# Kernel optimization log

Hardware: AMD Instinct MI355X
Metric: run time of the kernel (lower is better)

The kernel has to match this reference:

```python
import jax, jax.numpy as jnp
import numpy as np

E, H, PV, RD, NS, SP, T = 4, 64, 300, 64, 8, 6, 2
N = 5000
IN_GRU = 2 * E * H  # 512


def layer_norm(x, g, b, eps=1e-5):
    m = jnp.mean(x, axis=-1, keepdims=True)
    v = jnp.var(x, axis=-1, keepdims=True)
    return (x - m) * jax.lax.rsqrt(v + eps) * g + b


def setup_inputs() -> dict:
    key = jax.random.key(0)
    ks = jax.random.split(key, 32)
    s = 0.05
    inp = {
        'adjacency_matrix': (jax.random.uniform(ks[0], (E, N, N), jnp.float32) < 0.01).astype(jnp.float32),
        'node_states': jax.random.normal(ks[1], (N, NS), jnp.float32),
        'node_ids': jnp.arange(N, dtype=jnp.int32),
        'node_vectors': jax.random.normal(ks[2], (N, PV), jnp.float32),
        'node_size_and_pos': jax.random.normal(ks[3], (N, SP), jnp.float32),
        # reduce_dimentionality: Linear(300,64)+Tanh
        'W_red': jax.random.normal(ks[4], (PV, RD), jnp.float32) * s,
        'b_red': jnp.zeros((RD,), jnp.float32),
        # node_init2hidden: Linear(64+8+6,64)+Tanh
        'W_init': jax.random.normal(ks[5], (RD + NS + SP, H), jnp.float32) * s,
        'b_init': jnp.zeros((H,), jnp.float32),
        # per-edge-type message FCs (stacked over edge types)
        'W_out': jax.random.normal(ks[6], (E, H, H), jnp.float32) * s,
        'b_out': jnp.zeros((E, H), jnp.float32),
        'W_in_e': jax.random.normal(ks[7], (E, H, H), jnp.float32) * s,
        'b_in_e': jnp.zeros((E, H), jnp.float32),
        # LayerNormGRUCell(2*E*H, H)
        'W_ih_rz': jax.random.normal(ks[8], (IN_GRU, 2 * H), jnp.float32) * s,
        'b_ih_rz': jnp.zeros((2 * H,), jnp.float32),
        'W_hh_rz': jax.random.normal(ks[9], (H, 2 * H), jnp.float32) * s,
        'b_hh_rz': jnp.zeros((2 * H,), jnp.float32),
        'W_ih_c': jax.random.normal(ks[10], (IN_GRU, H), jnp.float32) * s,
        'b_ih_c': jnp.zeros((H,), jnp.float32),
        'W_hh_c': jax.random.normal(ks[11], (H, H), jnp.float32) * s,
        'b_hh_c': jnp.zeros((H,), jnp.float32),
        'g_i2h': jnp.ones((2 * H,), jnp.float32), 'be_i2h': jnp.zeros((2 * H,), jnp.float32),
        'g_h2h': jnp.ones((2 * H,), jnp.float32), 'be_h2h': jnp.zeros((2 * H,), jnp.float32),
        'g_ci': jnp.ones((H,), jnp.float32), 'be_ci': jnp.zeros((H,), jnp.float32),
        'g_ch': jnp.ones((H,), jnp.float32), 'be_ch': jnp.zeros((H,), jnp.float32),
    }
    return inp


def _messages(A, h, W, b):
    # per-edge-type FC + tanh: [E,N,H]
    hs = jnp.tanh(jnp.einsum('nh,ehk->enk', h, W) + b[:, None, :])
    # adjacency matmul per edge type: [E,N,N] @ [E,N,H] -> [E,N,H]
    m = jnp.einsum('enm,emh->enh', A, hs)
    # torch.stack(list,1).view(N,-1) == [N, E*H]
    return jnp.transpose(m, (1, 0, 2)).reshape(h.shape[0], E * H)


def reference(adjacency_matrix, node_states, node_ids, node_vectors, node_size_and_pos,
              W_red, b_red, W_init, b_init, W_out, b_out, W_in_e, b_in_e,
              W_ih_rz, b_ih_rz, W_hh_rz, b_hh_rz, W_ih_c, b_ih_c, W_hh_c, b_hh_c,
              g_i2h, be_i2h, g_h2h, be_h2h, g_ci, be_ci, g_ch, be_ch):
    emb = jnp.tanh(node_vectors @ W_red + b_red)                      # [N,RD]
    node_init = jnp.concatenate([emb, node_states, node_size_and_pos], axis=1)
    h = jnp.tanh(node_init @ W_init + b_init)                          # [N,H]
    A_out = adjacency_matrix
    A_in = jnp.transpose(adjacency_matrix, (0, 2, 1))
    for _ in range(T):
        m_out = _messages(A_out, h, W_out, b_out)                      # [N,E*H]
        m_in = _messages(A_in, h, W_in_e, b_in_e)                      # [N,E*H]
        msg = jnp.concatenate([m_out, m_in], axis=1)                   # [N,2EH]
        # LayerNormGRUCell
        rz = jax.nn.sigmoid(layer_norm(msg @ W_ih_rz + b_ih_rz, g_i2h, be_i2h)
                            + layer_norm(h @ W_hh_rz + b_hh_rz, g_h2h, be_h2h))
        r, z = rz[:, :H], rz[:, H:]
        c = jnp.tanh(layer_norm(msg @ W_ih_c + b_ih_c, g_ci, be_ci)
                     + r * layer_norm(h @ W_hh_c + b_hh_c, g_ch, be_ch))
        h = z * h + (1.0 - z) * c
    return h
```

## Files before the change

kernel.cpp:

```cpp
#include <hip/hip_runtime.h>
#include <math.h>

#define N    5000
#define E    4
#define H    64
#define PV   300
#define RD   64
#define NS_  8
#define SP_  6
#define NI   (RD + NS_ + SP_)
#define GH   (2 * H)
#define MSGW (2 * E * H)
#define CAP  128
#define NPB  8
#define MSG_BPS 256

#define PK_S0 ((MSGW / 4) * GH)
#define PK_S1 ((MSGW / 4) * H)
#define PK_S2 ((H / 4) * GH)
#define PK_S3 ((H / 4) * H)
#define PK_TOT (PK_S0 + PK_S1 + PK_S2 + PK_S3)

__device__ __forceinline__ float wsum(float v) {
    v += __shfl_xor(v, 32, 64);
    v += __shfl_xor(v, 16, 64);
    v += __shfl_xor(v, 8, 64);
    v += __shfl_xor(v, 4, 64);
    v += __shfl_xor(v, 2, 64);
    v += __shfl_xor(v, 1, 64);
    return v;
}

__global__ __launch_bounds__(256) void k_zero(int4* __restrict__ p) {
    const int i = blockIdx.x * 256 + threadIdx.x;
    if (i < (2 * E * N) / 4) p[i] = make_int4(0, 0, 0, 0);
}

__global__ __launch_bounds__(256) void k_pack(
    const float* __restrict__ Wih_rz, const float* __restrict__ Wih_c,
    const float* __restrict__ Whh_rz, const float* __restrict__ Whh_c,
    float4* __restrict__ Prz, float4* __restrict__ Pc,
    float4* __restrict__ Phrz, float4* __restrict__ Phc)
{
    const int i = blockIdx.x * 256 + threadIdx.x;
    if (i < PK_S0) {
        const int kq = i / GH, col = i - kq * GH;
        Prz[i] = make_float4(Wih_rz[(4 * kq + 0) * GH + col],
                             Wih_rz[(4 * kq + 1) * GH + col],
                             Wih_rz[(4 * kq + 2) * GH + col],
                             Wih_rz[(4 * kq + 3) * GH + col]);
    } else if (i < PK_S0 + PK_S1) {
        const int t = i - PK_S0;
        const int kq = t / H, col = t - kq * H;
        Pc[t] = make_float4(Wih_c[(4 * kq + 0) * H + col],
                            Wih_c[(4 * kq + 1) * H + col],
                            Wih_c[(4 * kq + 2) * H + col],
                            Wih_c[(4 * kq + 3) * H + col]);
    } else if (i < PK_S0 + PK_S1 + PK_S2) {
        const int t = i - PK_S0 - PK_S1;
        const int kq = t / GH, col = t - kq * GH;
        Phrz[t] = make_float4(Whh_rz[(4 * kq + 0) * GH + col],
                              Whh_rz[(4 * kq + 1) * GH + col],
                              Whh_rz[(4 * kq + 2) * GH + col],
                              Whh_rz[(4 * kq + 3) * GH + col]);
    } else if (i < PK_TOT) {
        const int t = i - PK_S0 - PK_S1 - PK_S2;
        const int kq = t / H, col = t - kq * H;
        Phc[t] = make_float4(Whh_c[(4 * kq + 0) * H + col],
                             Whh_c[(4 * kq + 1) * H + col],
                             Whh_c[(4 * kq + 2) * H + col],
                             Whh_c[(4 * kq + 3) * H + col]);
    }
}

__global__ __launch_bounds__(64) void k_init(
    const float* __restrict__ NV, const float* __restrict__ NSt,
    const float* __restrict__ SPos, const float* __restrict__ Wred,
    const float* __restrict__ bred, const float* __restrict__ Winit,
    const float* __restrict__ binit, float* __restrict__ h)
{
    __shared__ float nv[4 * PV];
    __shared__ float ni[4 * NI];
    const int n0 = blockIdx.x * 4;
    const int j = threadIdx.x;

    for (int idx = j; idx < 4 * PV; idx += 64) nv[idx] = NV[(size_t)n0 * PV + idx];
    __syncthreads();

    float acc[4];
    {
        const float br = bred[j];
        #pragma unroll
        for (int nn = 0; nn < 4; ++nn) acc[nn] = br;
    }
    for (int k = 0; k < PV; ++k) {
        const float w = Wred[k * RD + j];
        #pragma unroll
        for (int nn = 0; nn < 4; ++nn) acc[nn] += nv[nn * PV + k] * w;
    }
    #pragma unroll
    for (int nn = 0; nn < 4; ++nn) ni[nn * NI + j] = tanhf(acc[nn]);
    if (j < NS_) {
        #pragma unroll
        for (int nn = 0; nn < 4; ++nn) ni[nn * NI + RD + j] = NSt[(size_t)(n0 + nn) * NS_ + j];
    }
    if (j < SP_) {
        #pragma unroll
        for (int nn = 0; nn < 4; ++nn) ni[nn * NI + RD + NS_ + j] = SPos[(size_t)(n0 + nn) * SP_ + j];
    }
    __syncthreads();

    float a2[4];
    {
        const float bi = binit[j];
        #pragma unroll
        for (int nn = 0; nn < 4; ++nn) a2[nn] = bi;
    }
    for (int k = 0; k < NI; ++k) {
        const float w = Winit[k * H + j];
        #pragma unroll
        for (int nn = 0; nn < 4; ++nn) a2[nn] += ni[nn * NI + k] * w;
    }
    #pragma unroll
    for (int nn = 0; nn < 4; ++nn) h[(size_t)(n0 + nn) * H + j] = tanhf(a2[nn]);
}

__global__ __launch_bounds__(256) void k_build(
    const float* __restrict__ A, int* __restrict__ cnt_out, int* __restrict__ cnt_in,
    unsigned short* __restrict__ idx_out, unsigned short* __restrict__ idx_in)
{
    const int r = blockIdx.x;
    const int e = r / N;
    const int n = r - e * N;
    __shared__ int s_cnt;
    __shared__ int s_cols[CAP];
    if (threadIdx.x == 0) s_cnt = 0;
    __syncthreads();

    const float4* row = (const float4*)(A + (size_t)r * N);
    const int lane = threadIdx.x & 63;
    #pragma unroll
    for (int it = 0; it < 5; ++it) {
        const int c = threadIdx.x + it * 256;
        float4 v = make_float4(0.f, 0.f, 0.f, 0.f);
        if (c < N / 4) v = row[c];
        #pragma unroll
        for (int comp = 0; comp < 4; ++comp) {
            const float val = (comp == 0) ? v.x : (comp == 1) ? v.y : (comp == 2) ? v.z : v.w;
            const bool p = (val != 0.f);
            const unsigned long long m = __ballot(p);
            if (m) {
                int base = 0;
                if (lane == 0) base = atomicAdd(&s_cnt, (int)__popcll(m));
                base = __shfl(base, 0, 64);
                if (p) {
                    const int pos = base + (int)__popcll(m & ((1ull << lane) - 1ull));
                    if (pos < CAP) s_cols[pos] = 4 * c + comp;
                }
            }
        }
    }
    __syncthreads();
    const int cnt = min(s_cnt, CAP);
    if (threadIdx.x == 0) cnt_out[r] = cnt;
    for (int i = threadIdx.x; i < cnt; i += 256)
        idx_out[(size_t)r * CAP + i] = (unsigned short)s_cols[i];
    for (int i = threadIdx.x; i < cnt; i += 256) {
        const int m = s_cols[i];
        const int p = atomicAdd(&cnt_in[e * N + m], 1);
        if (p < CAP) idx_in[(size_t)(e * N + m) * CAP + p] = (unsigned short)n;
    }
}

__global__ __launch_bounds__(256) void k_hs(
    const float* __restrict__ h, const float* __restrict__ Wout,
    const float* __restrict__ bout, const float* __restrict__ Win,
    const float* __restrict__ bin, float* __restrict__ hs_out,
    float* __restrict__ hs_in)
{
    __shared__ float hsd[8 * H];
    const int n0 = blockIdx.x * 8;
    const int tid = threadIdx.x;
    const int e = tid >> 6, j = tid & 63;

    for (int idx = tid; idx < 8 * H; idx += 256) hsd[idx] = h[(size_t)n0 * H + idx];
    __syncthreads();

    float aO[8], aI[8];
    {
        const float bO = bout[e * H + j], bI = bin[e * H + j];
        #pragma unroll
        for (int nn = 0; nn < 8; ++nn) { aO[nn] = bO; aI[nn] = bI; }
    }
    for (int k = 0; k < H; ++k) {
        const float wo = Wout[(e * H + k) * H + j];
        const float wi = Win[(e * H + k) * H + j];
        #pragma unroll
        for (int nn = 0; nn < 8; ++nn) {
            const float hv = hsd[nn * H + k];
            aO[nn] += hv * wo;
            aI[nn] += hv * wi;
        }
    }
    #pragma unroll
    for (int nn = 0; nn < 8; ++nn) {
        hs_out[((size_t)e * N + n0 + nn) * H + j] = tanhf(aO[nn]);
        hs_in[((size_t)e * N + n0 + nn) * H + j]  = tanhf(aI[nn]);
    }
}

__global__ __launch_bounds__(256) void k_msg(
    const float* __restrict__ hs_out, const float* __restrict__ hs_in,
    const int* __restrict__ cnt_out, const int* __restrict__ cnt_in,
    const unsigned short* __restrict__ idx_out, const unsigned short* __restrict__ idx_in,
    float* __restrict__ msg)
{
    const int slice = blockIdx.x & 7;
    const int sb = blockIdx.x >> 3;
    const int dir = slice >> 2;
    const int e = slice & 3;
    const int tid = threadIdx.x;
    const int wv = tid >> 6;
    const int lane = tid & 63;
    const int g = lane >> 4;
    const int l = lane & 15;

    const float4* hs4 = (const float4*)((dir ? hs_in : hs_out) + (size_t)e * N * H);
    const int* cnt = (dir ? cnt_in : cnt_out) + e * N;
    const unsigned short* idx = (dir ? idx_in : idx_out) + (size_t)e * N * CAP;
    float4* mdst = (float4*)msg;

    for (int n = sb * 4 + wv; n < N; n += MSG_BPS * 4) {
        const int c = min(cnt[n], CAP);
        const unsigned short* lst = idx + (size_t)n * CAP;

        float ax = 0.f, ay = 0.f, az = 0.f, aw = 0.f;
        int i = g;
        for (; i + 12 < c; i += 16) {
            const int m0 = lst[i];
            const int m1 = lst[i + 4];
            const int m2 = lst[i + 8];
            const int m3 = lst[i + 12];
            const float4 v0 = hs4[(size_t)m0 * (H / 4) + l];
            const float4 v1 = hs4[(size_t)m1 * (H / 4) + l];
            const float4 v2 = hs4[(size_t)m2 * (H / 4) + l];
            const float4 v3 = hs4[(size_t)m3 * (H / 4) + l];
            ax += (v0.x + v1.x) + (v2.x + v3.x);
            ay += (v0.y + v1.y) + (v2.y + v3.y);
            az += (v0.z + v1.z) + (v2.z + v3.z);
            aw += (v0.w + v1.w) + (v2.w + v3.w);
        }
        for (; i < c; i += 4) {
            const float4 v = hs4[(size_t)lst[i] * (H / 4) + l];
            ax += v.x; ay += v.y; az += v.z; aw += v.w;
        }

        ax += __shfl_xor(ax, 16, 64); ay += __shfl_xor(ay, 16, 64);
        az += __shfl_xor(az, 16, 64); aw += __shfl_xor(aw, 16, 64);
        ax += __shfl_xor(ax, 32, 64); ay += __shfl_xor(ay, 32, 64);
        az += __shfl_xor(az, 32, 64); aw += __shfl_xor(aw, 32, 64);

        if (g == 0) {
            mdst[(size_t)n * (MSGW / 4) + dir * (E * H / 4) + e * (H / 4) + l] =
                make_float4(ax, ay, az, aw);
        }
    }
}

__global__ __launch_bounds__(256) void k_gru(
    const float* __restrict__ msg, const float* __restrict__ h,
    const float4* __restrict__ Prz, const float4* __restrict__ Pc,
    const float4* __restrict__ Phrz, const float4* __restrict__ Phc,
    const float* __restrict__ bih_rz, const float* __restrict__ bhh_rz,
    const float* __restrict__ bih_c, const float* __restrict__ bhh_c,
    const float* __restrict__ g_i2h, const float* __restrict__ be_i2h,
    const float* __restrict__ g_h2h, const float* __restrict__ be_h2h,
    const float* __restrict__ g_ci, const float* __restrict__ be_ci,
    const float* __restrict__ g_ch, const float* __restrict__ be_ch,
    float* __restrict__ h_out)
{
    __shared__ float pb[2][64][12];
    const int n0 = blockIdx.x * NPB;
    const int tid = threadIdx.x;
    const int j = tid & 63;
    const int wv = __builtin_amdgcn_readfirstlane(tid >> 6);
    const int kh = wv & 1;
    const int q  = wv >> 1;
    const int nb = q * 4;

    const float4* ms4 = (const float4*)msg;
    const float4* hg4 = (const float4*)h;

    float a0[4], a1[4], c0[4];
    {
        const float v0 = kh ? 0.f : bih_rz[j];
        const float v1 = kh ? 0.f : bih_rz[H + j];
        const float vc = kh ? 0.f : bih_c[j];
        #pragma unroll
        for (int i = 0; i < 4; ++i) { a0[i] = v0; a1[i] = v1; c0[i] = vc; }
    }
    {
        const int kq0 = kh * (MSGW / 8);
        #pragma unroll 2
        for (int t = 0; t < MSGW / 8; ++t) {
            const int kq = kq0 + t;
            const float4 w0 = Prz[kq * GH + j];
            const float4 w1 = Prz[kq * GH + 64 + j];
            const float4 wc = Pc[kq * H + j];
            #pragma unroll
            for (int i = 0; i < 4; ++i) {
                const float4 m = ms4[(size_t)(n0 + nb + i) * (MSGW / 4) + kq];
                a0[i] += m.x * w0.x; a0[i] += m.y * w0.y;
                a0[i] += m.z * w0.z; a0[i] += m.w * w0.w;
                a1[i] += m.x * w1.x; a1[i] += m.y * w1.y;
                a1[i] += m.z * w1.z; a1[i] += m.w * w1.w;
                c0[i] += m.x * wc.x; c0[i] += m.y * wc.y;
                c0[i] += m.z * wc.z; c0[i] += m.w * wc.w;
            }
        }
    }

    float b0[4], b1[4], ch[4];
    {
        const float v0 = kh ? 0.f : bhh_rz[j];
        const float v1 = kh ? 0.f : bhh_rz[H + j];
        const float vc = kh ? 0.f : bhh_c[j];
        #pragma unroll
        for (int i = 0; i < 4; ++i) { b0[i] = v0; b1[i] = v1; ch[i] = vc; }
    }
    {
        const int kq0 = kh * (H / 8);
        #pragma unroll 2
        for (int t = 0; t < H / 8; ++t) {
            const int kq = kq0 + t;
            const float4 w0 = Phrz[kq * GH + j];
            const float4 w1 = Phrz[kq * GH + 64 + j];
            const float4 wc = Phc[kq * H + j];
            #pragma unroll
            for (int i = 0; i < 4; ++i) {
                const float4 m = hg4[(size_t)(n0 + nb + i) * (H / 4) + kq];
                b0[i] += m.x * w0.x; b0[i] += m.y * w0.y;
                b0[i] += m.z * w0.z; b0[i] += m.w * w0.w;
                b1[i] += m.x * w1.x; b1[i] += m.y * w1.y;
                b1[i] += m.z * w1.z; b1[i] += m.w * w1.w;
                ch[i] += m.x * wc.x; ch[i] += m.y * wc.y;
                ch[i] += m.z * wc.z; ch[i] += m.w * wc.w;
            }
        }
    }

    if (kh == 1) {
        #pragma unroll
        for (int i = 0; i < 4; ++i) {
            pb[q][j][i]     = a0[i];
            pb[q][j][4 + i] = a1[i];
            pb[q][j][8 + i] = c0[i];
        }
    }
    __syncthreads();
    if (kh == 0) {
        #pragma unroll
        for (int i = 0; i < 4; ++i) {
            a0[i] += pb[q][j][i];
            a1[i] += pb[q][j][4 + i];
            c0[i] += pb[q][j][8 + i];
        }
    }
    __syncthreads();
    if (kh == 1) {
        #pragma unroll
        for (int i = 0; i < 4; ++i) {
            pb[q][j][i]     = b0[i];
            pb[q][j][4 + i] = b1[i];
            pb[q][j][8 + i] = ch[i];
        }
    }
    __syncthreads();

    if (kh == 0) {
        #pragma unroll
        for (int i = 0; i < 4; ++i) {
            b0[i] += pb[q][j][i];
            b1[i] += pb[q][j][4 + i];
            ch[i] += pb[q][j][8 + i];
        }

        const float gi0 = g_i2h[j], gi1 = g_i2h[H + j], bi0 = be_i2h[j], bi1 = be_i2h[H + j];
        const float gh0 = g_h2h[j], gh1 = g_h2h[H + j], bh0 = be_h2h[j], bh1 = be_h2h[H + j];
        const float gci = g_ci[j], bci = be_ci[j], gchv = g_ch[j], bchv = be_ch[j];

        #pragma unroll
        for (int i = 0; i < 4; ++i) {
            float s  = wsum(a0[i] + a1[i]);
            float q_ = wsum(a0[i] * a0[i] + a1[i] * a1[i]);
            float mn = s * (1.f / GH);
            float vr = q_ * (1.f / GH) - mn * mn;
            float rs = rsqrtf(vr + 1e-5f);
            float x0 = (a0[i] - mn) * rs * gi0 + bi0;
            float x1 = (a1[i] - mn) * rs * gi1 + bi1;
            float s2  = wsum(b0[i] + b1[i]);
            float q2  = wsum(b0[i] * b0[i] + b1[i] * b1[i]);
            float mn2 = s2 * (1.f / GH);
            float vr2 = q2 * (1.f / GH) - mn2 * mn2;
            float rs2 = rsqrtf(vr2 + 1e-5f);
            float y0 = (b0[i] - mn2) * rs2 * gh0 + bh0;
            float y1 = (b1[i] - mn2) * rs2 * gh1 + bh1;
            const float r_ = 1.f / (1.f + expf(-(x0 + y0)));
            const float z_ = 1.f / (1.f + expf(-(x1 + y1)));

            float s3  = wsum(c0[i]);
            float q3  = wsum(c0[i] * c0[i]);
            float mn3 = s3 * (1.f / H);
            float vr3 = q3 * (1.f / H) - mn3 * mn3;
            float rs3 = rsqrtf(vr3 + 1e-5f);
            float xc = (c0[i] - mn3) * rs3 * gci + bci;
            float s4  = wsum(ch[i]);
            float q4  = wsum(ch[i] * ch[i]);
            float mn4 = s4 * (1.f / H);
            float vr4 = q4 * (1.f / H) - mn4 * mn4;
            float rs4 = rsqrtf(vr4 + 1e-5f);
            float hc = (ch[i] - mn4) * rs4 * gchv + bchv;
            float c  = tanhf(xc + r_ * hc);
            const int n = n0 + nb + i;
            const float hp = h[(size_t)n * H + j];
            h_out[(size_t)n * H + j] = z_ * hp + (1.f - z_) * c;
        }
    }
}

extern "C" void kernel_launch(void* const* d_in, const int* in_sizes, int n_in,
                              void* d_out, int out_size, void* d_ws, size_t ws_size,
                              hipStream_t stream)
{
    const float* A      = (const float*)d_in[0];
    const float* nstate = (const float*)d_in[1];
    const float* nvec   = (const float*)d_in[3];
    const float* nsp    = (const float*)d_in[4];
    const float* Wred   = (const float*)d_in[5];
    const float* bred   = (const float*)d_in[6];
    const float* Winit  = (const float*)d_in[7];
    const float* binit  = (const float*)d_in[8];
    const float* Wout   = (const float*)d_in[9];
    const float* bout   = (const float*)d_in[10];
    const float* Wine   = (const float*)d_in[11];
    const float* bine   = (const float*)d_in[12];
    const float* Wih_rz = (const float*)d_in[13];
    const float* bih_rz = (const float*)d_in[14];
    const float* Whh_rz = (const float*)d_in[15];
    const float* bhh_rz = (const float*)d_in[16];
    const float* Wih_c  = (const float*)d_in[17];
    const float* bih_c  = (const float*)d_in[18];
    const float* Whh_c  = (const float*)d_in[19];
    const float* bhh_c  = (const float*)d_in[20];
    const float* g_i2h  = (const float*)d_in[21];
    const float* be_i2h = (const float*)d_in[22];
    const float* g_h2h  = (const float*)d_in[23];
    const float* be_h2h = (const float*)d_in[24];
    const float* g_ci   = (const float*)d_in[25];
    const float* be_ci  = (const float*)d_in[26];
    const float* g_ch   = (const float*)d_in[27];
    const float* be_ch  = (const float*)d_in[28];

    char* ws = (char*)d_ws;
    size_t off = 0;
    auto alloc = [&](size_t bytes) {
        void* p = ws + off;
        off += (bytes + 255) & ~(size_t)255;
        return p;
    };
    float* h0  = (float*)alloc((size_t)N * H * 4);
    float* h1  = (float*)alloc((size_t)N * H * 4);
    float* hsO = (float*)alloc((size_t)E * N * H * 4);
    float* hsI = (float*)alloc((size_t)E * N * H * 4);
    float* msg = (float*)alloc((size_t)N * MSGW * 4);
    int* cnts  = (int*)alloc((size_t)2 * E * N * 4);
    int* cnt_out = cnts;
    int* cnt_in  = cnts + E * N;
    unsigned short* idxO = (unsigned short*)alloc((size_t)E * N * CAP * 2);
    unsigned short* idxI = (unsigned short*)alloc((size_t)E * N * CAP * 2);
    float4* Prz  = (float4*)alloc((size_t)PK_S0 * 16);
    float4* Pc   = (float4*)alloc((size_t)PK_S1 * 16);
    float4* Phrz = (float4*)alloc((size_t)PK_S2 * 16);
    float4* Phc  = (float4*)alloc((size_t)PK_S3 * 16);

    k_zero<<<(2 * E * N / 4 + 255) / 256, 256, 0, stream>>>((int4*)cnts);
    k_pack<<<(PK_TOT + 255) / 256, 256, 0, stream>>>(Wih_rz, Wih_c, Whh_rz, Whh_c,
                                                     Prz, Pc, Phrz, Phc);
    k_init<<<N / 4, 64, 0, stream>>>(nvec, nstate, nsp, Wred, bred, Winit, binit, h0);
    k_build<<<E * N, 256, 0, stream>>>(A, cnt_out, cnt_in, idxO, idxI);

    const float* hc = h0;
    for (int t = 0; t < 2; ++t) {
        k_hs<<<N / 8, 256, 0, stream>>>(hc, Wout, bout, Wine, bine, hsO, hsI);
        k_msg<<<8 * MSG_BPS, 256, 0, stream>>>(hsO, hsI, cnt_out, cnt_in, idxO, idxI, msg);
        float* hn = (t == 1) ? (float*)d_out : h1;
        k_gru<<<(N + NPB - 1) / NPB, 256, 0, stream>>>(
            msg, hc, Prz, Pc, Phrz, Phc,
            bih_rz, bhh_rz, bih_c, bhh_c,
            g_i2h, be_i2h, g_h2h, be_h2h,
            g_ci, be_ci, g_ch, be_ch, hn);
        hc = hn;
    }
}
```

Before: 300.8 us.

## Merge setup kernels and fuse next-step edge transform into GRU kernel

Three setup kernels (zeroing the counts, packing the weights, node init) are merged into one launch that dispatches work by block range, and node init now handles 16 nodes per block. The second step's per-edge-type hidden transform (k_hs) is folded into the tail of the first GRU kernel, which keeps the new h in shared memory and computes the tanh(W h + b) outputs directly. k_build loads two float4s per iteration to raise memory-level parallelism. Together these cut kernel launches and one global round trip of h, at the cost of more work and shared memory per GRU block. The fused GRU path also relies on N being divisible by NPB.

```diff
diff --git a/kernel.cpp b/kernel.cpp
--- a/kernel.cpp
+++ b/kernel.cpp
@@ -21,6 +21,11 @@
 #define PK_S3 ((H / 4) * H)
 #define PK_TOT (PK_S0 + PK_S1 + PK_S2 + PK_S3)
 
+#define PRE_PACK_B 108
+#define PRE_ZERO_B 40
+#define PRE_INIT_B 313
+#define PRE_GRID (PRE_PACK_B + PRE_ZERO_B + PRE_INIT_B)
+
 __device__ __forceinline__ float wsum(float v) {
     v += __shfl_xor(v, 32, 64);
     v += __shfl_xor(v, 16, 64);
@@ -31,98 +36,113 @@
     return v;
 }
 
-__global__ __launch_bounds__(256) void k_zero(int4* __restrict__ p) {
-    const int i = blockIdx.x * 256 + threadIdx.x;
-    if (i < (2 * E * N) / 4) p[i] = make_int4(0, 0, 0, 0);
-}
-
-__global__ __launch_bounds__(256) void k_pack(
+__global__ __launch_bounds__(256) void k_pre(
     const float* __restrict__ Wih_rz, const float* __restrict__ Wih_c,
     const float* __restrict__ Whh_rz, const float* __restrict__ Whh_c,
     float4* __restrict__ Prz, float4* __restrict__ Pc,
-    float4* __restrict__ Phrz, float4* __restrict__ Phc)
-{
-    const int i = blockIdx.x * 256 + threadIdx.x;
-    if (i < PK_S0) {
-        const int kq = i / GH, col = i - kq * GH;
-        Prz[i] = make_float4(Wih_rz[(4 * kq + 0) * GH + col],
-                             Wih_rz[(4 * kq + 1) * GH + col],
-                             Wih_rz[(4 * kq + 2) * GH + col],
-                             Wih_rz[(4 * kq + 3) * GH + col]);
-    } else if (i < PK_S0 + PK_S1) {
-        const int t = i - PK_S0;
-        const int kq = t / H, col = t - kq * H;
-        Pc[t] = make_float4(Wih_c[(4 * kq + 0) * H + col],
-                            Wih_c[(4 * kq + 1) * H + col],
-                            Wih_c[(4 * kq + 2) * H + col],
-                            Wih_c[(4 * kq + 3) * H + col]);
-    } else if (i < PK_S0 + PK_S1 + PK_S2) {
-        const int t = i - PK_S0 - PK_S1;
-        const int kq = t / GH, col = t - kq * GH;
-        Phrz[t] = make_float4(Whh_rz[(4 * kq + 0) * GH + col],
-                              Whh_rz[(4 * kq + 1) * GH + col],
-                              Whh_rz[(4 * kq + 2) * GH + col],
-                              Whh_rz[(4 * kq + 3) * GH + col]);
-    } else if (i < PK_TOT) {
-        const int t = i - PK_S0 - PK_S1 - PK_S2;
-        const int kq = t / H, col = t - kq * H;
-        Phc[t] = make_float4(Whh_c[(4 * kq + 0) * H + col],
-                             Whh_c[(4 * kq + 1) * H + col],
-                             Whh_c[(4 * kq + 2) * H + col],
-                             Whh_c[(4 * kq + 3) * H + col]);
-    }
-}
-
-__global__ __launch_bounds__(64) void k_init(
+    float4* __restrict__ Phrz, float4* __restrict__ Phc,
+    int4* __restrict__ cnts,
     const float* __restrict__ NV, const float* __restrict__ NSt,
     const float* __restrict__ SPos, const float* __restrict__ Wred,
     const float* __restrict__ bred, const float* __restrict__ Winit,
     const float* __restrict__ binit, float* __restrict__ h)
 {
-    __shared__ float nv[4 * PV];
-    __shared__ float ni[4 * NI];
-    const int n0 = blockIdx.x * 4;
-    const int j = threadIdx.x;
-
-    for (int idx = j; idx < 4 * PV; idx += 64) nv[idx] = NV[(size_t)n0 * PV + idx];
-    __syncthreads();
-
-    float acc[4];
-    {
-        const float br = bred[j];
-        #pragma unroll
-        for (int nn = 0; nn < 4; ++nn) acc[nn] = br;
-    }
-    for (int k = 0; k < PV; ++k) {
-        const float w = Wred[k * RD + j];
-        #pragma unroll
-        for (int nn = 0; nn < 4; ++nn) acc[nn] += nv[nn * PV + k] * w;
-    }
-    #pragma unroll
-    for (int nn = 0; nn < 4; ++nn) ni[nn * NI + j] = tanhf(acc[nn]);
-    if (j < NS_) {
-        #pragma unroll
-        for (int nn = 0; nn < 4; ++nn) ni[nn * NI + RD + j] = NSt[(size_t)(n0 + nn) * NS_ + j];
-    }
-    if (j < SP_) {
-        #pragma unroll
-        for (int nn = 0; nn < 4; ++nn) ni[nn * NI + RD + NS_ + j] = SPos[(size_t)(n0 + nn) * SP_ + j];
-    }
-    __syncthreads();
-
-    float a2[4];
-    {
-        const float bi = binit[j];
-        #pragma unroll
-        for (int nn = 0; nn < 4; ++nn) a2[nn] = bi;
-    }
-    for (int k = 0; k < NI; ++k) {
-        const float w = Winit[k * H + j];
-        #pragma unroll
-        for (int nn = 0; nn < 4; ++nn) a2[nn] += ni[nn * NI + k] * w;
-    }
-    #pragma unroll
-    for (int nn = 0; nn < 4; ++nn) h[(size_t)(n0 + nn) * H + j] = tanhf(a2[nn]);
+    __shared__ float nv[16 * PV];
+    __shared__ float ni[16 * NI];
+    const int b = blockIdx.x;
+    const int tid = threadIdx.x;
+
+    if (b < PRE_PACK_B) {
+        const int i = b * 256 + tid;
+        if (i < PK_S0) {
+            const int kq = i / GH, col = i - kq * GH;
+            Prz[i] = make_float4(Wih_rz[(4 * kq + 0) * GH + col],
+                                 Wih_rz[(4 * kq + 1) * GH + col],
+                                 Wih_rz[(4 * kq + 2) * GH + col],
+                                 Wih_rz[(4 * kq + 3) * GH + col]);
+        } else if (i < PK_S0 + PK_S1) {
+            const int t = i - PK_S0;
+            const int kq = t / H, col = t - kq * H;
+            Pc[t] = make_float4(Wih_c[(4 * kq + 0) * H + col],
+                                Wih_c[(4 * kq + 1) * H + col],
+                                Wih_c[(4 * kq + 2) * H + col],
+                                Wih_c[(4 * kq + 3) * H + col]);
+        } else if (i < PK_S0 + PK_S1 + PK_S2) {
+            const int t = i - PK_S0 - PK_S1;
+            const int kq = t / GH, col = t - kq * GH;
+            Phrz[t] = make_float4(Whh_rz[(4 * kq + 0) * GH + col],
+                                  Whh_rz[(4 * kq + 1) * GH + col],
+                                  Whh_rz[(4 * kq + 2) * GH + col],
+                                  Whh_rz[(4 * kq + 3) * GH + col]);
+        } else {
+            const int t = i - PK_S0 - PK_S1 - PK_S2;
+            const int kq = t / H, col = t - kq * H;
+            Phc[t] = make_float4(Whh_c[(4 * kq + 0) * H + col],
+                                 Whh_c[(4 * kq + 1) * H + col],
+                                 Whh_c[(4 * kq + 2) * H + col],
+                                 Whh_c[(4 * kq + 3) * H + col]);
+        }
+    } else if (b < PRE_PACK_B + PRE_ZERO_B) {
+        const int i = (b - PRE_PACK_B) * 256 + tid;
+        if (i < (2 * E * N) / 4) cnts[i] = make_int4(0, 0, 0, 0);
+    } else {
+        const int n0 = (b - PRE_PACK_B - PRE_ZERO_B) * 16;
+        const int j = tid & 63;
+        const int w = tid >> 6;
+        const int nb = w * 4;
+
+        for (int idx = tid; idx < 16 * PV; idx += 256) {
+            const int n = n0 + idx / PV;
+            nv[idx] = (n < N) ? NV[(size_t)n0 * PV + idx] : 0.f;
+        }
+        __syncthreads();
+
+        float acc[4];
+        {
+            const float br = bred[j];
+            #pragma unroll
+            for (int nn = 0; nn < 4; ++nn) acc[nn] = br;
+        }
+        for (int k = 0; k < PV; ++k) {
+            const float wg = Wred[k * RD + j];
+            #pragma unroll
+            for (int nn = 0; nn < 4; ++nn) acc[nn] += nv[(nb + nn) * PV + k] * wg;
+        }
+        #pragma unroll
+        for (int nn = 0; nn < 4; ++nn) ni[(nb + nn) * NI + j] = tanhf(acc[nn]);
+        if (j < NS_) {
+            #pragma unroll
+            for (int nn = 0; nn < 4; ++nn) {
+                const int n = n0 + nb + nn;
+                ni[(nb + nn) * NI + RD + j] = (n < N) ? NSt[(size_t)n * NS_ + j] : 0.f;
+            }
+        }
+        if (j < SP_) {
+            #pragma unroll
+            for (int nn = 0; nn < 4; ++nn) {
+                const int n = n0 + nb + nn;
+                ni[(nb + nn) * NI + RD + NS_ + j] = (n < N) ? SPos[(size_t)n * SP_ + j] : 0.f;
+            }
+        }
+        __syncthreads();
+
+        float a2[4];
+        {
+            const float bi = binit[j];
+            #pragma unroll
+            for (int nn = 0; nn < 4; ++nn) a2[nn] = bi;
+        }
+        for (int k = 0; k < NI; ++k) {
+            const float wg = Winit[k * H + j];
+            #pragma unroll
+            for (int nn = 0; nn < 4; ++nn) a2[nn] += ni[(nb + nn) * NI + k] * wg;
+        }
+        #pragma unroll
+        for (int nn = 0; nn < 4; ++nn) {
+            const int n = n0 + nb + nn;
+            if (n < N) h[(size_t)n * H + j] = tanhf(a2[nn]);
+        }
+    }
 }
 
 __global__ __launch_bounds__(256) void k_build(
@@ -140,22 +160,30 @@
     const float4* row = (const float4*)(A + (size_t)r * N);
     const int lane = threadIdx.x & 63;
     #pragma unroll
-    for (int it = 0; it < 5; ++it) {
-        const int c = threadIdx.x + it * 256;
-        float4 v = make_float4(0.f, 0.f, 0.f, 0.f);
-        if (c < N / 4) v = row[c];
-        #pragma unroll
-        for (int comp = 0; comp < 4; ++comp) {
-            const float val = (comp == 0) ? v.x : (comp == 1) ? v.y : (comp == 2) ? v.z : v.w;
-            const bool p = (val != 0.f);
-            const unsigned long long m = __ballot(p);
-            if (m) {
-                int base = 0;
-                if (lane == 0) base = atomicAdd(&s_cnt, (int)__popcll(m));
-                base = __shfl(base, 0, 64);
-                if (p) {
-                    const int pos = base + (int)__popcll(m & ((1ull << lane) - 1ull));
-                    if (pos < CAP) s_cols[pos] = 4 * c + comp;
+    for (int it = 0; it < 3; ++it) {
+        const int c0 = threadIdx.x + it * 512;
+        const int c1 = c0 + 256;
+        float4 v0 = make_float4(0.f, 0.f, 0.f, 0.f);
+        float4 v1 = make_float4(0.f, 0.f, 0.f, 0.f);
+        if (c0 < N / 4) v0 = row[c0];
+        if (c1 < N / 4) v1 = row[c1];
+        #pragma unroll
+        for (int half = 0; half < 2; ++half) {
+            const float4 v = half ? v1 : v0;
+            const int c = half ? c1 : c0;
+            #pragma unroll
+            for (int comp = 0; comp < 4; ++comp) {
+                const float val = (comp == 0) ? v.x : (comp == 1) ? v.y : (comp == 2) ? v.z : v.w;
+                const bool p = (val != 0.f);
+                const unsigned long long m = __ballot(p);
+                if (m) {
+                    int base = 0;
+                    if (lane == 0) base = atomicAdd(&s_cnt, (int)__popcll(m));
+                    base = __shfl(base, 0, 64);
+                    if (p) {
+                        const int pos = base + (int)__popcll(m & ((1ull << lane) - 1ull));
+                        if (pos < CAP) s_cols[pos] = 4 * c + comp;
+                    }
                 }
             }
         }
@@ -277,9 +305,14 @@
     const float* __restrict__ g_h2h, const float* __restrict__ be_h2h,
     const float* __restrict__ g_ci, const float* __restrict__ be_ci,
     const float* __restrict__ g_ch, const float* __restrict__ be_ch,
-    float* __restrict__ h_out)
+    float* __restrict__ h_out,
+    const float* __restrict__ Wout, const float* __restrict__ bout,
+    const float* __restrict__ Win, const float* __restrict__ bin,
+    float* __restrict__ hs_out, float* __restrict__ hs_in,
+    const int write_hs)
 {
     __shared__ float pb[2][64][12];
+    __shared__ float hn[NPB][H];
     const int n0 = blockIdx.x * NPB;
     const int tid = threadIdx.x;
     const int j = tid & 63;
@@ -423,7 +456,35 @@
             float c  = tanhf(xc + r_ * hc);
             const int n = n0 + nb + i;
             const float hp = h[(size_t)n * H + j];
-            h_out[(size_t)n * H + j] = z_ * hp + (1.f - z_) * c;
+            const float hv = z_ * hp + (1.f - z_) * c;
+            h_out[(size_t)n * H + j] = hv;
+            hn[nb + i][j] = hv;
+        }
+    }
+    __syncthreads();
+
+    if (write_hs) {
+        const int e = wv;
+        float aO[8], aI[8];
+        {
+            const float bO = bout[e * H + j], bI = bin[e * H + j];
+            #pragma unroll
+            for (int nn = 0; nn < 8; ++nn) { aO[nn] = bO; aI[nn] = bI; }
+        }
+        for (int k = 0; k < H; ++k) {
+            const float wo = Wout[(e * H + k) * H + j];
+            const float wi = Win[(e * H + k) * H + j];
+            #pragma unroll
+            for (int nn = 0; nn < 8; ++nn) {
+                const float hv = hn[nn][k];
+                aO[nn] += hv * wo;
+                aI[nn] += hv * wi;
+            }
+        }
+        #pragma unroll
+        for (int nn = 0; nn < 8; ++nn) {
+            hs_out[((size_t)e * N + n0 + nn) * H + j] = tanhf(aO[nn]);
+            hs_in[((size_t)e * N + n0 + nn) * H + j]  = tanhf(aI[nn]);
         }
     }
 }
@@ -483,22 +544,25 @@
     float4* Phrz = (float4*)alloc((size_t)PK_S2 * 16);
     float4* Phc  = (float4*)alloc((size_t)PK_S3 * 16);
 
-    k_zero<<<(2 * E * N / 4 + 255) / 256, 256, 0, stream>>>((int4*)cnts);
-    k_pack<<<(PK_TOT + 255) / 256, 256, 0, stream>>>(Wih_rz, Wih_c, Whh_rz, Whh_c,
-                                                     Prz, Pc, Phrz, Phc);
-    k_init<<<N / 4, 64, 0, stream>>>(nvec, nstate, nsp, Wred, bred, Winit, binit, h0);
+    k_pre<<<PRE_GRID, 256, 0, stream>>>(Wih_rz, Wih_c, Whh_rz, Whh_c,
+                                        Prz, Pc, Phrz, Phc, (int4*)cnts,
+                                        nvec, nstate, nsp, Wred, bred, Winit, binit, h0);
     k_build<<<E * N, 256, 0, stream>>>(A, cnt_out, cnt_in, idxO, idxI);
-
-    const float* hc = h0;
-    for (int t = 0; t < 2; ++t) {
-        k_hs<<<N / 8, 256, 0, stream>>>(hc, Wout, bout, Wine, bine, hsO, hsI);
-        k_msg<<<8 * MSG_BPS, 256, 0, stream>>>(hsO, hsI, cnt_out, cnt_in, idxO, idxI, msg);
-        float* hn = (t == 1) ? (float*)d_out : h1;
-        k_gru<<<(N + NPB - 1) / NPB, 256, 0, stream>>>(
-            msg, hc, Prz, Pc, Phrz, Phc,
-            bih_rz, bhh_rz, bih_c, bhh_c,
-            g_i2h, be_i2h, g_h2h, be_h2h,
-            g_ci, be_ci, g_ch, be_ch, hn);
-        hc = hn;
-    }
-}
+    k_hs<<<N / 8, 256, 0, stream>>>(h0, Wout, bout, Wine, bine, hsO, hsI);
+
+    k_msg<<<8 * MSG_BPS, 256, 0, stream>>>(hsO, hsI, cnt_out, cnt_in, idxO, idxI, msg);
+    k_gru<<<N / NPB, 256, 0, stream>>>(
+        msg, h0, Prz, Pc, Phrz, Phc,
+        bih_rz, bhh_rz, bih_c, bhh_c,
+        g_i2h, be_i2h, g_h2h, be_h2h,
+        g_ci, be_ci, g_ch, be_ch, h1,
+        Wout, bout, Wine, bine, hsO, hsI, 1);
+
+    k_msg<<<8 * MSG_BPS, 256, 0, stream>>>(hsO, hsI, cnt_out, cnt_in, idxO, idxI, msg);
+    k_gru<<<N / NPB, 256, 0, stream>>>(
+        msg, h1, Prz, Pc, Phrz, Phc,
+        bih_rz, bhh_rz, bih_c, bhh_c,
+        g_i2h, be_i2h, g_h2h, be_h2h,
+        g_ci, be_ci, g_ch, be_ch, (float*)d_out,
+        Wout, bout, Wine, bine, hsO, hsI, 0);
+}
```

Result: faster. 282.3 us (-6.1%).
